# Kernel optimization log

Hardware: AMD Instinct MI355X
Metric: run time of the kernel (lower is better)

## Reference

```python
import jax, jax.numpy as jnp
from jax import lax
import numpy as np

WINDOW = 51
HALF = WINDOW // 2  # 25
K_SAUVOLA = 0.2     # skimage threshold_sauvola default k
RGB_W = np.array([0.2989, 0.5870, 0.1140], dtype=np.float32)  # tf.image.rgb_to_grayscale weights


def _window_sum(x, axis):
    """Sliding-window sum of length WINDOW along `axis`, 'same' size, reflect padding.
    O(1) per pixel via cumulative sums (integral-image style), matching the
    uniform_filter-based local statistics in skimage's Sauvola."""
    pad = [(0, 0)] * x.ndim
    pad[axis] = (HALF, HALF)
    xp = jnp.pad(x, pad, mode='reflect')
    cs = jnp.cumsum(xp, axis=axis)
    zshape = list(cs.shape)
    zshape[axis] = 1
    cs = jnp.concatenate([jnp.zeros(zshape, cs.dtype), cs], axis=axis)
    n = cs.shape[axis]
    hi = lax.slice_in_dim(cs, WINDOW, n, axis=axis)
    lo = lax.slice_in_dim(cs, 0, n - WINDOW, axis=axis)
    return hi - lo


def _box_mean(x):
    # separable 51x51 box filter over H (axis 1) and W (axis 2)
    s = _window_sum(_window_sum(x, axis=1), axis=2)
    return s / jnp.asarray(WINDOW * WINDOW, x.dtype)


def setup_inputs() -> dict:
    key = jax.random.key(0)
    inputs = jax.random.uniform(key, (8, 1024, 1024, 3), dtype=jnp.float32)
    return {"inputs": inputs}


def reference(inputs) -> jnp.ndarray:
    # RGB -> grayscale (channels == 3 branch), keep channel dim [B,H,W,1]
    gray = jnp.einsum('bhwc,c->bhw', inputs, jnp.asarray(RGB_W))[..., None]
    # local mean / std over 51x51 window
    m = _box_mean(gray)
    m2 = _box_mean(gray * gray)
    var = jnp.maximum(m2 - m * m, 0.0)
    s = jnp.sqrt(var)
    # skimage default dynamic range: r = 0.5 * (max - min) over the whole array
    r = 0.5 * (jnp.max(gray) - jnp.min(gray))
    thresh = m * (1.0 + K_SAUVOLA * (s / r - 1.0))
    # (gray > thresh) * 1
    return (gray > thresh).astype(jnp.float32)
```

## Files before the change

### kernel.cpp

```cpp
#include <hip/hip_runtime.h>

#define IMW 1024
#define IMH 1024
#define NB  8
#define HALF 25
#define STRIP 64
#define NCELL 64

#define W_R ((double)0.2989f)
#define W_G ((double)0.5870f)
#define W_B ((double)0.1140f)
#define INV_AREA (1.0 / 2601.0)

__device__ __forceinline__ int refl(int i, int n) {
    if (i < 0) i = -i;
    if (i >= n) i = 2 * n - 2 - i;
    return i;
}

__device__ __forceinline__ double wsum(const double* __restrict__ C, int p) {
    int a = p + HALF; if (a > IMW - 1) a = IMW - 1;
    int b = p - HALF - 1;
    double s = C[a] - (b >= 0 ? C[b] : 0.0);
    if (p <= HALF - 1)      s += C[HALF - p] - C[0];
    if (p >= IMW - HALF)    s += C[IMW - 2] - C[2*IMW - 2 - HALF - 1 - p];
    return s;
}

__global__ void k0_init(unsigned long long* cells) {
    cells[threadIdx.x] = ~0ULL;
    cells[NCELL + threadIdx.x] = 0ULL;
}

__global__ __launch_bounds__(256) void k1_rowpass(const float* __restrict__ in,
                                                  double2* __restrict__ hp,
                                                  unsigned long long* __restrict__ cells) {
    __shared__ double cs1[IMW];
    __shared__ double cs2[IMW];
    __shared__ double wt1[4], wt2[4], bmin[4], bmax[4];
    const int row = blockIdx.x;
    const long long base = (long long)row * IMW;
    const int t = threadIdx.x;
    const int lane = t & 63, w = t >> 6;

    const float4* p4 = (const float4*)(in + base * 3);
    float4 f0 = p4[3*t], f1 = p4[3*t+1], f2 = p4[3*t+2];
    double g0 = (double)f0.x*W_R + (double)f0.y*W_G + (double)f0.z*W_B;
    double g1 = (double)f0.w*W_R + (double)f1.x*W_G + (double)f1.y*W_B;
    double g2 = (double)f1.z*W_R + (double)f1.w*W_G + (double)f2.x*W_B;
    double g3 = (double)f2.y*W_R + (double)f2.z*W_G + (double)f2.w*W_B;

    double l1_0 = g0, l1_1 = l1_0 + g1, l1_2 = l1_1 + g2, l1_3 = l1_2 + g3;
    double q0 = g0*g0, q1 = g1*g1, q2 = g2*g2, q3 = g3*g3;
    double l2_0 = q0, l2_1 = l2_0 + q1, l2_2 = l2_1 + q2, l2_3 = l2_2 + q3;

    double lmin = fmin(fmin(g0, g1), fmin(g2, g3));
    double lmax = fmax(fmax(g0, g1), fmax(g2, g3));
    for (int off = 32; off; off >>= 1) {
        lmin = fmin(lmin, __shfl_down(lmin, off));
        lmax = fmax(lmax, __shfl_down(lmax, off));
    }
    if (lane == 0) { bmin[w] = lmin; bmax[w] = lmax; }

    double v1 = l1_3, v2 = l2_3;
    for (int off = 1; off < 64; off <<= 1) {
        double u1 = __shfl_up(v1, off);
        double u2 = __shfl_up(v2, off);
        if (lane >= off) { v1 += u1; v2 += u2; }
    }
    if (lane == 63) { wt1[w] = v1; wt2[w] = v2; }
    __syncthreads();
    double e1 = v1 - l1_3, e2 = v2 - l2_3;
    for (int j = 0; j < w; j++) { e1 += wt1[j]; e2 += wt2[j]; }

    double2* c1 = (double2*)&cs1[4*t];
    double2* c2 = (double2*)&cs2[4*t];
    c1[0] = make_double2(e1 + l1_0, e1 + l1_1);
    c1[1] = make_double2(e1 + l1_2, e1 + l1_3);
    c2[0] = make_double2(e2 + l2_0, e2 + l2_1);
    c2[1] = make_double2(e2 + l2_2, e2 + l2_3);

    if (t == 0) {
        double m0 = fmin(fmin(bmin[0], bmin[1]), fmin(bmin[2], bmin[3]));
        double m1 = fmax(fmax(bmax[0], bmax[1]), fmax(bmax[2], bmax[3]));
        int cell = row & (NCELL - 1);
        atomicMin(&cells[cell], (unsigned long long)__double_as_longlong(m0));
        atomicMax(&cells[NCELL + cell], (unsigned long long)__double_as_longlong(m1));
    }
    __syncthreads();

    for (int k = 0; k < 4; k++) {
        int p = t + 256 * k;
        hp[base + p] = make_double2(wsum(cs1, p), wsum(cs2, p));
    }
}

__global__ __launch_bounds__(256) void k2_colpass(const float* __restrict__ in,
                                                  const double2* __restrict__ hp,
                                                  const unsigned long long* __restrict__ cells,
                                                  float* __restrict__ out) {
    __shared__ double sr[2];
    const int t = threadIdx.x;
    if (t < 64) {
        unsigned long long mn = cells[t];
        unsigned long long mx = cells[NCELL + t];
        for (int off = 32; off; off >>= 1) {
            unsigned long long a = __shfl_down(mn, off);
            unsigned long long b = __shfl_down(mx, off);
            mn = (a < mn) ? a : mn;
            mx = (b > mx) ? b : mx;
        }
        if (t == 0) {
            sr[0] = __longlong_as_double((long long)mn);
            sr[1] = __longlong_as_double((long long)mx);
        }
    }
    __syncthreads();
    const double r  = 0.5 * (sr[1] - sr[0]);
    const double r2 = r * r;

    const int id   = blockIdx.x;
    const int b    = id & 7;
    const int rest = id >> 3;
    const int ys   = rest & 15;
    const int xc   = rest >> 4;
    const int x  = xc * 256 + t;
    const int y0 = ys * STRIP;
    const long long ib = (long long)b * IMH * IMW;

    double2 v = make_double2(0.0, 0.0);
    #pragma unroll 8
    for (int j = -HALF; j <= HALF; j++) {
        int ry = refl(y0 + j, IMH);
        double2 h = hp[ib + (long long)ry * IMW + x];
        v.x += h.x; v.y += h.y;
    }

    #pragma unroll 8
    for (int y = y0; y < y0 + STRIP; y++) {
        long long pix = ib + (long long)y * IMW + x;
        const float* p = in + pix * 3;
        double g = (double)p[0]*W_R + (double)p[1]*W_G + (double)p[2]*W_B;

        double m  = v.x * INV_AREA;
        double va = fmax(v.y * INV_AREA - m * m, 0.0);
        double A  = g - 0.8 * m;
        int o = (A > 0.0) && (A * A * r2 > 0.04 * m * m * va);
        out[pix] = o ? 1.0f : 0.0f;

        int ra = refl(y + HALF + 1, IMH);
        int rs = refl(y - HALF, IMH);
        double2 ha = hp[ib + (long long)ra * IMW + x];
        double2 hs = hp[ib + (long long)rs * IMW + x];
        v.x += ha.x - hs.x;
        v.y += ha.y - hs.y;
    }
}

extern "C" void kernel_launch(void* const* d_in, const int* in_sizes, int n_in,
                              void* d_out, int out_size, void* d_ws, size_t ws_size,
                              hipStream_t stream) {
    const float* in = (const float*)d_in[0];
    float* out = (float*)d_out;

    unsigned long long* cells = (unsigned long long*)d_ws;
    double2* hp = (double2*)((char*)d_ws + 4096);

    hipLaunchKernelGGL(k0_init, dim3(1), dim3(NCELL), 0, stream, cells);
    hipLaunchKernelGGL(k1_rowpass, dim3(NB * IMH), dim3(256), 0, stream,
                       in, hp, cells);
    hipLaunchKernelGGL(k2_colpass, dim3((IMW / 256) * (IMH / STRIP) * NB), dim3(256), 0, stream,
                       in, hp, cells, out);
}
```

Baseline: 235.8 us.

## Store horizontal sums as float, cache grayscale, and halve column strip height

The row pass now writes its horizontal window sums as float2 instead of double2, halving the intermediate buffer traffic. It also stores a float grayscale plane, so the column pass reads 4 bytes per pixel instead of re-reading 12 bytes of RGB. Strip height drops from 64 to 32, doubling the block count for more parallelism at the cost of more redundant window warm-up reads. Rounding the sums to float can flip threshold decisions for pixels near the threshold.

```diff
diff --git a/kernel.cpp b/kernel.cpp
--- a/kernel.cpp
+++ b/kernel.cpp
@@ -4,7 +4,7 @@
 #define IMH 1024
 #define NB  8
 #define HALF 25
-#define STRIP 64
+#define STRIP 32
 #define NCELL 64
 
 #define W_R ((double)0.2989f)
@@ -33,7 +33,8 @@
 }
 
 __global__ __launch_bounds__(256) void k1_rowpass(const float* __restrict__ in,
-                                                  double2* __restrict__ hp,
+                                                  float2* __restrict__ hp,
+                                                  float* __restrict__ gray,
                                                   unsigned long long* __restrict__ cells) {
     __shared__ double cs1[IMW];
     __shared__ double cs2[IMW];
@@ -49,6 +50,8 @@
     double g1 = (double)f0.w*W_R + (double)f1.x*W_G + (double)f1.y*W_B;
     double g2 = (double)f1.z*W_R + (double)f1.w*W_G + (double)f2.x*W_B;
     double g3 = (double)f2.y*W_R + (double)f2.z*W_G + (double)f2.w*W_B;
+
+    ((float4*)(gray + base))[t] = make_float4((float)g0, (float)g1, (float)g2, (float)g3);
 
     double l1_0 = g0, l1_1 = l1_0 + g1, l1_2 = l1_1 + g2, l1_3 = l1_2 + g3;
     double q0 = g0*g0, q1 = g1*g1, q2 = g2*g2, q3 = g3*g3;
@@ -91,12 +94,12 @@
 
     for (int k = 0; k < 4; k++) {
         int p = t + 256 * k;
-        hp[base + p] = make_double2(wsum(cs1, p), wsum(cs2, p));
+        hp[base + p] = make_float2((float)wsum(cs1, p), (float)wsum(cs2, p));
     }
 }
 
-__global__ __launch_bounds__(256) void k2_colpass(const float* __restrict__ in,
-                                                  const double2* __restrict__ hp,
+__global__ __launch_bounds__(256) void k2_colpass(const float* __restrict__ gray,
+                                                  const float2* __restrict__ hp,
                                                   const unsigned long long* __restrict__ cells,
                                                   float* __restrict__ out) {
     __shared__ double sr[2];
@@ -122,38 +125,37 @@
     const int id   = blockIdx.x;
     const int b    = id & 7;
     const int rest = id >> 3;
-    const int ys   = rest & 15;
-    const int xc   = rest >> 4;
+    const int ys   = rest & 31;
+    const int xc   = rest >> 5;
     const int x  = xc * 256 + t;
     const int y0 = ys * STRIP;
     const long long ib = (long long)b * IMH * IMW;
 
-    double2 v = make_double2(0.0, 0.0);
+    double vx = 0.0, vy = 0.0;
     #pragma unroll 8
     for (int j = -HALF; j <= HALF; j++) {
         int ry = refl(y0 + j, IMH);
-        double2 h = hp[ib + (long long)ry * IMW + x];
-        v.x += h.x; v.y += h.y;
+        float2 h = hp[ib + (long long)ry * IMW + x];
+        vx += (double)h.x; vy += (double)h.y;
     }
 
     #pragma unroll 8
     for (int y = y0; y < y0 + STRIP; y++) {
         long long pix = ib + (long long)y * IMW + x;
-        const float* p = in + pix * 3;
-        double g = (double)p[0]*W_R + (double)p[1]*W_G + (double)p[2]*W_B;
+        double g = (double)gray[pix];
 
-        double m  = v.x * INV_AREA;
-        double va = fmax(v.y * INV_AREA - m * m, 0.0);
+        double m  = vx * INV_AREA;
+        double va = fmax(vy * INV_AREA - m * m, 0.0);
         double A  = g - 0.8 * m;
         int o = (A > 0.0) && (A * A * r2 > 0.04 * m * m * va);
         out[pix] = o ? 1.0f : 0.0f;
 
         int ra = refl(y + HALF + 1, IMH);
         int rs = refl(y - HALF, IMH);
-        double2 ha = hp[ib + (long long)ra * IMW + x];
-        double2 hs = hp[ib + (long long)rs * IMW + x];
-        v.x += ha.x - hs.x;
-        v.y += ha.y - hs.y;
+        float2 ha = hp[ib + (long long)ra * IMW + x];
+        float2 hs = hp[ib + (long long)rs * IMW + x];
+        vx += (double)ha.x - (double)hs.x;
+        vy += (double)ha.y - (double)hs.y;
     }
 }
 
@@ -164,11 +166,13 @@
     float* out = (float*)d_out;
 
     unsigned long long* cells = (unsigned long long*)d_ws;
-    double2* hp = (double2*)((char*)d_ws + 4096);
+    float2* hp = (float2*)((char*)d_ws + 4096);
+    float* gray = (float*)((char*)d_ws + 4096
+                           + (size_t)NB * IMH * IMW * sizeof(float2));
 
     hipLaunchKernelGGL(k0_init, dim3(1), dim3(NCELL), 0, stream, cells);
     hipLaunchKernelGGL(k1_rowpass, dim3(NB * IMH), dim3(256), 0, stream,
-                       in, hp, cells);
+                       in, hp, gray, cells);
     hipLaunchKernelGGL(k2_colpass, dim3((IMW / 256) * (IMH / STRIP) * NB), dim3(256), 0, stream,
-                       in, hp, cells, out);
+                       gray, hp, cells, out);
 }
```

New measurement: 206.5 us. 12.5% less time.
